# Optimization experiments

Measured on AMD Instinct MI355X. Metric: run time of the kernel, lower is better.

## Reference

```python
import jax, jax.numpy as jnp
import numpy as np
import math

B, N, D, H, L = 2, 512, 256, 8, 3
EPS = 1e-4


def setup_inputs() -> dict:
    key = jax.random.key(0)
    ks = jax.random.split(key, 16)
    # valid boxes (x1, y1, x2, y2) with positive width/height
    xy = jax.random.uniform(ks[0], (B, N, 2), dtype=jnp.float32) * 800.0
    wh = jax.random.uniform(ks[1], (B, N, 2), dtype=jnp.float32) * 200.0 + 1.0
    boxes = jnp.concatenate([xy, xy + wh], axis=-1)
    features = jax.random.normal(ks[2], (B, N, D), dtype=jnp.float32)
    mask = jnp.ones((B, N, N), dtype=jnp.int32)
    s = 1.0 / math.sqrt(D)
    Wq = jax.random.normal(ks[3], (L, D, D), dtype=jnp.float32) * s
    Wk = jax.random.normal(ks[4], (L, D, D), dtype=jnp.float32) * s
    Wv = jax.random.normal(ks[5], (L, D, D), dtype=jnp.float32) * s
    Wo = jax.random.normal(ks[6], (L, D, D), dtype=jnp.float32) * s
    Wg = jax.random.normal(ks[7], (L, D, H), dtype=jnp.float32) * s
    bq = jnp.zeros((L, D), jnp.float32)
    bk = jnp.zeros((L, D), jnp.float32)
    bv = jnp.zeros((L, D), jnp.float32)
    bo = jnp.zeros((L, D), jnp.float32)
    bg = jnp.zeros((L, H), jnp.float32)
    feat_range = jnp.arange(D // 8, dtype=jnp.float32)
    div_mat = jnp.power(1000.0, (8.0 / D) * feat_range) / 100.0
    return dict(boxes=boxes, features=features, mask=mask,
                Wq=Wq, bq=bq, Wk=Wk, bk=bk, Wv=Wv, bv=bv, Wo=Wo, bo=bo,
                Wg=Wg, bg=bg, div_mat=div_mat)


def _position_embedding(boxes, div_mat):
    # relative geometry between all box pairs (q == k == boxes)
    cx = (boxes[..., 0] + boxes[..., 2]) / 2
    cy = (boxes[..., 1] + boxes[..., 3]) / 2
    w = jnp.maximum(boxes[..., 2] - boxes[..., 0], EPS)
    h = jnp.maximum(boxes[..., 3] - boxes[..., 1], EPS)
    rel_x = jnp.log(jnp.abs(cx[:, None, :] - cx[:, :, None]) / w[:, None, :] + EPS)
    rel_y = jnp.log(jnp.abs(cy[:, None, :] - cy[:, :, None]) / h[:, None, :] + EPS)
    rel_w = jnp.log(w[:, :, None] / w[:, None, :] + EPS)
    rel_h = jnp.log(h[:, :, None] / h[:, None, :] + EPS)
    rel = jnp.stack([rel_x, rel_y, rel_w, rel_h], axis=-1)  # (B,N,N,4)
    pm = rel[..., None] / div_mat                            # (B,N,N,4,D/8)
    emb = jnp.concatenate([jnp.sin(pm), jnp.cos(pm)], axis=-1)  # (B,N,N,4,D/4)
    return emb.reshape(*emb.shape[:3], -1)                   # (B,N,N,D)


def reference(boxes, features, mask, Wq, bq, Wk, bk, Wv, bv, Wo, bo, Wg, bg, div_mat):
    emb = _position_embedding(boxes, div_mat)  # (B,N,N,D)
    dh = D // H
    inv_sqrt_dk = 1.0 / math.sqrt(dh)
    mask_b = (mask[:, None, :, :] == 0)  # (B,1,N,N)
    x = features

    def heads(t):  # (B,N,D) -> (B,H,N,dh)
        return t.reshape(B, N, H, dh).transpose(0, 2, 1, 3)

    for l in range(L):
        q = jax.nn.relu(x @ Wq[l] + bq[l])
        k = jax.nn.relu(x @ Wk[l] + bk[l])
        v = jax.nn.relu(x @ Wv[l] + bv[l])
        qh, kh, vh = heads(q), heads(k), heads(v)
        geo = jax.nn.relu(emb @ Wg[l] + bg[l])           # (B,N,N,H)
        geo = geo.transpose(0, 3, 1, 2)                   # (B,H,N,N)
        scores = jnp.einsum('bhqd,bhkd->bhqk', qh, kh) * inv_sqrt_dk
        scores = scores + jnp.log(geo + 1e-6)
        scores = jnp.where(mask_b, -1e9, scores)
        atten = jax.nn.softmax(scores, axis=-1)
        y = jnp.einsum('bhqk,bhkd->bhqd', atten, vh)      # (B,H,N,dh)
        y = y.transpose(0, 2, 1, 3).reshape(B, N, D)
        y = jax.nn.relu(y @ Wo[l] + bo[l])
        x = x + y
    return x
```

## Files before the change

### kernel.cpp

```cpp
#include <hip/hip_runtime.h>
#include <hip/hip_fp16.h>

#define BB 2
#define NNq 512
#define DDm 256
#define HHh 8
#define DHh 32
#define LLn 3

static constexpr float EPSF   = 1e-4f;
static constexpr float INV2PI = 0.15915494309189535f;
static constexpr float SCALE  = 0.17677669529663687f;

#if __has_builtin(__builtin_amdgcn_fractf)
#define FRACTF(x) __builtin_amdgcn_fractf(x)
#else
#define FRACTF(x) ((x) - floorf(x))
#endif
#if __has_builtin(__builtin_amdgcn_sinf)
#define SINR(x) __builtin_amdgcn_sinf(x)
#define COSR(x) __builtin_amdgcn_cosf(x)
#else
#define SINR(x) __sinf((x) * 6.2831853071795865f)
#define COSR(x) __cosf((x) * 6.2831853071795865f)
#endif

typedef _Float16 f16x8 __attribute__((ext_vector_type(8)));
typedef _Float16 f16x4 __attribute__((ext_vector_type(4)));
typedef _Float16 f16x2 __attribute__((ext_vector_type(2)));
typedef float    f32x4 __attribute__((ext_vector_type(4)));

__device__ inline f16x2 pk2(float a, float b) {
#if __has_builtin(__builtin_amdgcn_cvt_pkrtz)
    return __builtin_bit_cast(f16x2, __builtin_amdgcn_cvt_pkrtz(a, b));
#else
    f16x2 r; r[0] = (_Float16)a; r[1] = (_Float16)b; return r;
#endif
}
union U16x8 { f16x8 v; f16x2 h[4]; };

__global__ __launch_bounds__(256) void k_wcvt(const float* __restrict__ Wq,
        const float* __restrict__ Wk, const float* __restrict__ Wv,
        const float* __restrict__ Wo, _Float16* __restrict__ WT) {
    __shared__ _Float16 t[64][72];
    const int tid = threadIdx.x;
    const int mat = blockIdx.z;
    const int l = mat >> 2, op = mat & 3;
    const float* W = (op == 0 ? Wq : op == 1 ? Wk : op == 2 ? Wv : Wo)
                     + (size_t)l * 65536;
    const int k0 = blockIdx.x * 64, n0 = blockIdx.y * 64;
    for (int u = tid; u < 64 * 16; u += 256) {
        int k = u >> 4, n4 = (u & 15) * 4;
        float4 w4 = *reinterpret_cast<const float4*>(&W[(size_t)(k0 + k) * 256 + n0 + n4]);
        t[n4 + 0][k] = (_Float16)w4.x; t[n4 + 1][k] = (_Float16)w4.y;
        t[n4 + 2][k] = (_Float16)w4.z; t[n4 + 3][k] = (_Float16)w4.w;
    }
    __syncthreads();
    for (int u = tid; u < 64 * 8; u += 256) {
        int n = u >> 3, kc = (u & 7) * 8;
        *reinterpret_cast<f16x8*>(&WT[((size_t)mat * 256 + n0 + n) * 256 + k0 + kc]) =
            *reinterpret_cast<const f16x8*>(&t[n][kc]);
    }
}

__global__ __launch_bounds__(256) void k_geo(const float* __restrict__ boxes,
                                             const float* __restrict__ Wg,
                                             const float* __restrict__ bg,
                                             const float* __restrict__ divm,
                                             const int* __restrict__ maskp,
                                             __half* __restrict__ lg) {
    __shared__ char smem[16384];
    _Float16* WgT = reinterpret_cast<_Float16*>(smem);
    __half (*obuf)[24][68] = reinterpret_cast<__half (*)[24][68]>(smem);

    const int tid = threadIdx.x;
    for (int idx = tid; idx < 32 * 256; idx += 256) {
        int n = idx >> 8, k = idx & 255;
        float w = (n < 24) ? Wg[(size_t)(n >> 3) * 2048 + (size_t)k * 8 + (n & 7)] : 0.f;
        WgT[n * 256 + (k ^ ((n & 7) << 3))] = (_Float16)w;
    }
    __syncthreads();

    const int lane = tid & 63;
    const int wid  = tid >> 6;
    const int ln15 = lane & 15;
    const int kgrp = lane >> 4;

    float invd[8];
    {
        const float4* dv4 = reinterpret_cast<const float4*>(divm);
        float4 da = dv4[kgrp * 2], db = dv4[kgrp * 2 + 1];
        invd[0] = INV2PI / da.x; invd[1] = INV2PI / da.y;
        invd[2] = INV2PI / da.z; invd[3] = INV2PI / da.w;
        invd[4] = INV2PI / db.x; invd[5] = INV2PI / db.y;
        invd[6] = INV2PI / db.z; invd[7] = INV2PI / db.w;
    }
    const int n0 = ln15;
    const int n1 = 16 + ln15;
    const float bg0 = bg[n0];
    const float bg1 = (n1 < 24) ? bg[n1] : 0.f;

    const int mask  = (ln15 & 7) << 3;
    const int flip5 = mask & 32;
    const int kb    = (kgrp << 3) ^ (mask & 24);
    const int base0 = n0 * 256 + kb;
    const int base1 = n1 * 256 + kb;

    f16x8 bS0[4], bC0[4], bS1[4], bC1[4];
#pragma unroll
    for (int kc2 = 0; kc2 < 4; ++kc2) {
        const int koffS = ((2 * kc2) * 32) ^ flip5;
        const int koffC = ((2 * kc2 + 1) * 32) ^ flip5;
        bS0[kc2] = *reinterpret_cast<const f16x8*>(&WgT[base0 + koffS]);
        bC0[kc2] = *reinterpret_cast<const f16x8*>(&WgT[base0 + koffC]);
        bS1[kc2] = *reinterpret_cast<const f16x8*>(&WgT[base1 + koffS]);
        bC1[kc2] = *reinterpret_cast<const f16x8*>(&WgT[base1 + koffC]);
    }
    __syncthreads();

    const float4* boxes4 = reinterpret_cast<const float4*>(boxes);
    const size_t plane = (size_t)NNq * NNq;

    const int base4 = (blockIdx.x * 4 + wid) * 4;
#pragma unroll
    for (int it = 0; it < 4; ++it) {
        const int slab = base4 + it;
        const int p0 = slab << 4;
        const int b  = p0 >> 18;
        const int rem = p0 & (NNq * NNq - 1);
        const int i  = rem >> 9;
        const int j0 = rem & (NNq - 1);

        float4 Bi = boxes4[b * NNq + i];
        float4 Bj = boxes4[b * NNq + j0 + ln15];
        float cxi = 0.5f * (Bi.x + Bi.z), cyi = 0.5f * (Bi.y + Bi.w);
        float wi  = fmaxf(Bi.z - Bi.x, EPSF), hi = fmaxf(Bi.w - Bi.y, EPSF);
        float cxj = 0.5f * (Bj.x + Bj.z), cyj = 0.5f * (Bj.y + Bj.w);
        float wj  = fmaxf(Bj.z - Bj.x, EPSF), hj = fmaxf(Bj.w - Bj.y, EPSF);
        float rel[4];
        rel[0] = __logf(fabsf(cxj - cxi) / wj + EPSF);
        rel[1] = __logf(fabsf(cyj - cyi) / hj + EPSF);
        rel[2] = __logf(wi / wj + EPSF);
        rel[3] = __logf(hi / hj + EPSF);

        f32x4 acc0 = {0.f, 0.f, 0.f, 0.f};
        f32x4 acc1 = {0.f, 0.f, 0.f, 0.f};

#pragma unroll
        for (int kc2 = 0; kc2 < 4; ++kc2) {
            const float rc = rel[kc2];
            U16x8 afs, afc;
#pragma unroll
            for (int jj = 0; jj < 4; ++jj) {
                float rv0 = FRACTF(rc * invd[2 * jj]);
                float rv1 = FRACTF(rc * invd[2 * jj + 1]);
                afs.h[jj] = pk2(SINR(rv0), SINR(rv1));
                afc.h[jj] = pk2(COSR(rv0), COSR(rv1));
            }
            acc0 = __builtin_amdgcn_mfma_f32_16x16x32_f16(afs.v, bS0[kc2], acc0, 0, 0, 0);
            acc0 = __builtin_amdgcn_mfma_f32_16x16x32_f16(afc.v, bC0[kc2], acc0, 0, 0, 0);
            acc1 = __builtin_amdgcn_mfma_f32_16x16x32_f16(afs.v, bS1[kc2], acc1, 0, 0, 0);
            acc1 = __builtin_amdgcn_mfma_f32_16x16x32_f16(afc.v, bC1[kc2], acc1, 0, 0, 0);
        }

#pragma unroll
        for (int r = 0; r < 4; ++r) {
            const int m = it * 16 + (kgrp << 2) + r;
            float g0 = fmaxf(acc0[r] + bg0, 0.f);
            obuf[wid][n0][m] = __float2half(g0);
            if (n1 < 24) {
                float g1 = fmaxf(acc1[r] + bg1, 0.f);
                obuf[wid][n1][m] = __float2half(g1);
            }
        }
    }
    __syncthreads();

    const int b_  = base4 >> 14;
    const int i_  = (base4 >> 5) & (NNq - 1);
    const int j0b = (base4 & 31) << 4;
    const int mv  = maskp[((size_t)b_ * NNq + i_) * NNq + j0b + lane];
    size_t obase = (size_t)b_ * plane + (size_t)i_ * NNq + j0b + lane;
#pragma unroll
    for (int t = 0; t < 24; ++t) {
        float g = __half2float(obuf[wid][t][lane]);
        float v = (mv != 0) ? __logf(g + 1e-6f) : -60000.0f;
        lg[obase + (size_t)t * (BB * plane)] = __float2half(v);
    }
}

#define LDP 264
__global__ __launch_bounds__(256) void k_gemm_qkv(const float* __restrict__ A,
        const _Float16* __restrict__ WT0, const _Float16* __restrict__ WT1,
        const _Float16* __restrict__ WT2,
        const float* __restrict__ b0, const float* __restrict__ b1, const float* __restrict__ b2,
        _Float16* __restrict__ C0, _Float16* __restrict__ C1, _Float16* __restrict__ C2) {
    const _Float16* WTz = (blockIdx.z == 0) ? WT0 : (blockIdx.z == 1) ? WT1 : WT2;
    const float*    bia = (blockIdx.z == 0) ? b0 : (blockIdx.z == 1) ? b1 : b2;
    _Float16*       C   = (blockIdx.z == 0) ? C0 : (blockIdx.z == 1) ? C1 : C2;

    __shared__ _Float16 As[32 * LDP];
    __shared__ _Float16 Ws[64 * LDP];

    const int tid = threadIdx.x;
    const int m0 = blockIdx.x * 32, n0 = blockIdx.y * 64;

    for (int u = tid; u < 32 * 64; u += 256) {
        int m = u >> 6, k4 = (u & 63) * 4;
        float4 av = *reinterpret_cast<const float4*>(&A[(size_t)(m0 + m) * 256 + k4]);
        f16x4 hv = {(_Float16)av.x, (_Float16)av.y, (_Float16)av.z, (_Float16)av.w};
        *reinterpret_cast<f16x4*>(&As[m * LDP + k4]) = hv;
    }
    for (int u = tid; u < 2048; u += 256) {
        int n = u >> 5, kc = (u & 31) * 8;
        *reinterpret_cast<f16x8*>(&Ws[n * LDP + kc]) =
            *reinterpret_cast<const f16x8*>(&WTz[(size_t)(n0 + n) * 256 + kc]);
    }
    __syncthreads();

    const int lane = tid & 63;
    const int wid  = tid >> 6;
    const int ln15 = lane & 15;
    const int kgrp = lane >> 4;
    const int mw   = (wid & 1) * 16;
    const int nsel = (wid >> 1) * 16;
    const int kfr  = kgrp * 8;

    f32x4 acc[2] = {{0.f,0.f,0.f,0.f},{0.f,0.f,0.f,0.f}};
#pragma unroll
    for (int kc = 0; kc < 8; ++kc) {
        f16x8 af = *reinterpret_cast<const f16x8*>(&As[(mw + ln15) * LDP + kc * 32 + kfr]);
#pragma unroll
        for (int t = 0; t < 2; ++t) {
            f16x8 bf = *reinterpret_cast<const f16x8*>(
                &Ws[(nsel + t * 32 + ln15) * LDP + kc * 32 + kfr]);
            acc[t] = __builtin_amdgcn_mfma_f32_16x16x32_f16(af, bf, acc[t], 0, 0, 0);
        }
    }

#pragma unroll
    for (int t = 0; t < 2; ++t) {
        const int col = n0 + nsel + t * 32 + ln15;
        const float bv = bia[col];
#pragma unroll
        for (int r = 0; r < 4; ++r) {
            const int row = m0 + mw + kgrp * 4 + r;
            C[(size_t)row * 256 + col] = (_Float16)fmaxf(acc[t][r] + bv, 0.f);
        }
    }
}

__global__ __launch_bounds__(256) void k_gemm_o(const _Float16* __restrict__ A,
        const _Float16* __restrict__ WT0,
        const float* __restrict__ bia,
        float* __restrict__ C, const float* __restrict__ resid) {
    __shared__ _Float16 As[32 * LDP];
    __shared__ _Float16 Ws[64 * LDP];

    const int tid = threadIdx.x;
    const int m0 = blockIdx.x * 32, n0 = blockIdx.y * 64;

    for (int u = tid; u < 1024; u += 256) {
        int m = u >> 5, kc = (u & 31) * 8;
        *reinterpret_cast<f16x8*>(&As[m * LDP + kc]) =
            *reinterpret_cast<const f16x8*>(&A[(size_t)(m0 + m) * 256 + kc]);
    }
    for (int u = tid; u < 2048; u += 256) {
        int n = u >> 5, kc = (u & 31) * 8;
        *reinterpret_cast<f16x8*>(&Ws[n * LDP + kc]) =
            *reinterpret_cast<const f16x8*>(&WT0[(size_t)(n0 + n) * 256 + kc]);
    }
    __syncthreads();

    const int lane = tid & 63;
    const int wid  = tid >> 6;
    const int ln15 = lane & 15;
    const int kgrp = lane >> 4;
    const int mw   = (wid & 1) * 16;
    const int nsel = (wid >> 1) * 16;
    const int kfr  = kgrp * 8;

    f32x4 acc[2] = {{0.f,0.f,0.f,0.f},{0.f,0.f,0.f,0.f}};
#pragma unroll
    for (int kc = 0; kc < 8; ++kc) {
        f16x8 af = *reinterpret_cast<const f16x8*>(&As[(mw + ln15) * LDP + kc * 32 + kfr]);
#pragma unroll
        for (int t = 0; t < 2; ++t) {
            f16x8 bf = *reinterpret_cast<const f16x8*>(
                &Ws[(nsel + t * 32 + ln15) * LDP + kc * 32 + kfr]);
            acc[t] = __builtin_amdgcn_mfma_f32_16x16x32_f16(af, bf, acc[t], 0, 0, 0);
        }
    }

#pragma unroll
    for (int t = 0; t < 2; ++t) {
        const int col = n0 + nsel + t * 32 + ln15;
        const float bv = bia[col];
#pragma unroll
        for (int r = 0; r < 4; ++r) {
            const int row = m0 + mw + kgrp * 4 + r;
            float o = fmaxf(acc[t][r] + bv, 0.f) + resid[(size_t)row * 256 + col];
            C[(size_t)row * 256 + col] = o;
        }
    }
}

__global__ __launch_bounds__(256) void k_attn(const _Float16* __restrict__ q,
                                              const _Float16* __restrict__ kk,
                                              const _Float16* __restrict__ vv,
                                              const __half* __restrict__ lg,
                                              _Float16* __restrict__ y, int l) {
    __shared__ _Float16 Kh[512 * 32];
    __shared__ _Float16 VT[32 * 512];
    __shared__ _Float16 Ps[4][16 * 128];

    const int bh = blockIdx.y;
    const int b = bh >> 3, h = bh & 7;
    const int i0t = blockIdx.x * 16;

    const int tid  = threadIdx.x;
    const int lane = tid & 63, wid = tid >> 6;
    const int ln15 = lane & 15, kgrp = lane >> 4;

    for (int u = tid; u < 2048; u += 256) {
        int j = u >> 2, d8 = (u & 3) * 8;
        const size_t src = (size_t)(b * NNq + j) * DDm + h * DHh + d8;
        f16x8 kv = *reinterpret_cast<const f16x8*>(&kk[src]);
        *reinterpret_cast<f16x8*>(reinterpret_cast<char*>(Kh) +
            ((j * 64 + d8 * 2) ^ ((j & 7) << 4))) = kv;
        f16x8 v8 = *reinterpret_cast<const f16x8*>(&vv[src]);
#pragma unroll
        for (int e = 0; e < 8; ++e) {
            int row = d8 + e;
            *reinterpret_cast<_Float16*>(reinterpret_cast<char*>(VT) +
                ((row * 1024 + j * 2) ^ ((row & 7) << 4))) = v8[e];
        }
    }

    f16x8 qf = *reinterpret_cast<const f16x8*>(
        &q[(size_t)(b * NNq + i0t + ln15) * DDm + h * DHh + kgrp * 8]);
    __syncthreads();

    const int jbase = wid * 128;
    const size_t plane = (size_t)NNq * NNq;
    const size_t lg_base = (size_t)((l * 8 + h) * BB + b) * plane;

    f32x4 s[8];
#pragma unroll
    for (int t = 0; t < 8; ++t) {
        int j = jbase + t * 16 + ln15;
        f16x8 kf = *reinterpret_cast<const f16x8*>(reinterpret_cast<char*>(Kh) +
            ((j * 64 + kgrp * 16) ^ ((j & 7) << 4)));
        f32x4 z = {0.f, 0.f, 0.f, 0.f};
        s[t] = __builtin_amdgcn_mfma_f32_16x16x32_f16(qf, kf, z, 0, 0, 0);
    }

#pragma unroll
    for (int t = 0; t < 8; ++t) {
        const size_t jg = jbase + t * 16 + ln15;
#pragma unroll
        for (int r = 0; r < 4; ++r) {
            float lgv = __half2float(lg[lg_base + (size_t)(i0t + kgrp * 4 + r) * NNq + jg]);
            s[t][r] = s[t][r] * SCALE + lgv;
        }
    }

    float m_[4], l_[4];
#pragma unroll
    for (int r = 0; r < 4; ++r) {
        float mx = s[0][r];
#pragma unroll
        for (int t = 1; t < 8; ++t) mx = fmaxf(mx, s[t][r]);
#pragma unroll
        for (int o = 1; o < 16; o <<= 1) mx = fmaxf(mx, __shfl_xor(mx, o, 64));
        float sum = 0.f;
#pragma unroll
        for (int t = 0; t < 8; ++t) {
            float p = __expf(s[t][r] - mx);
            s[t][r] = p; sum += p;
        }
#pragma unroll
        for (int o = 1; o < 16; o <<= 1) sum += __shfl_xor(sum, o, 64);
        m_[r] = mx; l_[r] = sum;
    }

    {
        char* psb = reinterpret_cast<char*>(Ps[wid]);
#pragma unroll
        for (int r = 0; r < 4; ++r) {
            const int row = kgrp * 4 + r;
            const int rb = row * 256, sw = (row & 7) << 4;
#pragma unroll
            for (int t = 0; t < 8; ++t) {
                int byte = (rb + (t * 16 + ln15) * 2) ^ sw;
                *reinterpret_cast<_Float16*>(psb + byte) = (_Float16)s[t][r];
            }
        }
    }

    f32x4 oacc[2] = {{0.f,0.f,0.f,0.f},{0.f,0.f,0.f,0.f}};
    {
        char* psb = reinterpret_cast<char*>(Ps[wid]);
#pragma unroll
        for (int kc = 0; kc < 4; ++kc) {
            f16x8 pf = *reinterpret_cast<const f16x8*>(psb +
                ((ln15 * 256 + kc * 64 + kgrp * 16) ^ ((ln15 & 7) << 4)));
#pragma unroll
            for (int dt = 0; dt < 2; ++dt) {
                int d = dt * 16 + ln15;
                f16x8 vf = *reinterpret_cast<const f16x8*>(reinterpret_cast<char*>(VT) +
                    ((d * 1024 + (jbase + kc * 32 + kgrp * 8) * 2) ^ ((d & 7) << 4)));
                oacc[dt] = __builtin_amdgcn_mfma_f32_16x16x32_f16(pf, vf, oacc[dt], 0, 0, 0);
            }
        }
    }

    {
        float* Op = reinterpret_cast<float*>(reinterpret_cast<char*>(Kh) + wid * 8192);
#pragma unroll
        for (int dt = 0; dt < 2; ++dt)
#pragma unroll
            for (int r = 0; r < 4; ++r)
                Op[(kgrp * 4 + r) * 32 + dt * 16 + ln15] = oacc[dt][r];
        if (ln15 == 0) {
#pragma unroll
            for (int r = 0; r < 4; ++r) {
                Op[512 + kgrp * 4 + r] = m_[r];
                Op[528 + kgrp * 4 + r] = l_[r];
            }
        }
    }
    __syncthreads();

    {
        const int i = tid >> 4, d0 = (tid & 15) * 2;
        float mw[4], M = -3.0e38f;
#pragma unroll
        for (int w = 0; w < 4; ++w) {
            mw[w] = reinterpret_cast<float*>(reinterpret_cast<char*>(Kh) + w * 8192)[512 + i];
            M = fmaxf(M, mw[w]);
        }
        float o0 = 0.f, o1 = 0.f, ls = 0.f;
#pragma unroll
        for (int w = 0; w < 4; ++w) {
            float* Op = reinterpret_cast<float*>(reinterpret_cast<char*>(Kh) + w * 8192);
            float sc = __expf(mw[w] - M);
            ls += Op[528 + i] * sc;
            o0 += Op[i * 32 + d0] * sc;
            o1 += Op[i * 32 + d0 + 1] * sc;
        }
        float inv = 1.0f / ls;
        f16x2 ov; ov[0] = (_Float16)(o0 * inv); ov[1] = (_Float16)(o1 * inv);
        *reinterpret_cast<f16x2*>(&y[(size_t)(b * NNq + i0t + i) * DDm + h * DHh + d0]) = ov;
    }
}

extern "C" void kernel_launch(void* const* d_in, const int* in_sizes, int n_in,
                              void* d_out, int out_size, void* d_ws, size_t ws_size,
                              hipStream_t stream) {
    const float* boxes    = (const float*)d_in[0];
    const float* features = (const float*)d_in[1];
    const int*   mask     = (const int*)d_in[2];
    const float* Wq = (const float*)d_in[3];
    const float* bq = (const float*)d_in[4];
    const float* Wk = (const float*)d_in[5];
    const float* bk = (const float*)d_in[6];
    const float* Wv = (const float*)d_in[7];
    const float* bv = (const float*)d_in[8];
    const float* Wo = (const float*)d_in[9];
    const float* bo = (const float*)d_in[10];
    const float* Wg = (const float*)d_in[11];
    const float* bg = (const float*)d_in[12];
    const float* dv = (const float*)d_in[13];

    char* ws = (char*)d_ws;
    __half*    lg = (__half*)(ws);
    _Float16*  WT = (_Float16*)(ws + 25165824);
    _Float16*  qb = (_Float16*)(ws + 26738688);
    _Float16*  kb = (_Float16*)(ws + 27262976);
    _Float16*  vb = (_Float16*)(ws + 27787264);
    _Float16*  yb = (_Float16*)(ws + 28311552);
    float*     x  = (float*)d_out;

    k_wcvt<<<dim3(4, 4, 12), dim3(256), 0, stream>>>(Wq, Wk, Wv, Wo, WT);
    k_geo<<<dim3(2048), dim3(256), 0, stream>>>(boxes, Wg, bg, dv, mask, lg);

    for (int l = 0; l < LLn; ++l) {
        const _Float16* WTq = WT + (size_t)(l * 4 + 0) * 65536;
        const _Float16* WTk = WT + (size_t)(l * 4 + 1) * 65536;
        const _Float16* WTv = WT + (size_t)(l * 4 + 2) * 65536;
        const _Float16* WTo = WT + (size_t)(l * 4 + 3) * 65536;
        const float* bq_l = bq + (size_t)l * DDm;
        const float* bk_l = bk + (size_t)l * DDm;
        const float* bv_l = bv + (size_t)l * DDm;
        const float* bo_l = bo + (size_t)l * DDm;
        const float* xin  = (l == 0) ? features : x;

        k_gemm_qkv<<<dim3(32, 4, 3), dim3(256), 0, stream>>>(
            xin, WTq, WTk, WTv, bq_l, bk_l, bv_l, qb, kb, vb);
        k_attn<<<dim3(32, 16), dim3(256), 0, stream>>>(qb, kb, vb, lg, yb, l);
        k_gemm_o<<<dim3(32, 4), dim3(256), 0, stream>>>(
            yb, WTo, bo_l, x, xin);
    }
}
```

Baseline: 118.6 us.

## Multiply softmax by geometry weight instead of adding its log; precompute Wg transpose once

The geometry kernel now stores relu(geo)+1e-6 (or zero for masked pairs) instead of its logarithm. The attention kernel multiplies exp(scaled score - max) by that weight, which removes a log per geometry element and an add per score. The per-block Wg transpose and conversion to fp16 moves into the weight-conversion kernel as an extra grid slice, and k_geo now reads the transposed weights from global memory with launch bounds raised to 4 blocks per unit. The risk is precision: the max no longer includes the log term, and storing the small weights in fp16 can underflow, though that matters little because the weight multiplies the probability. The max is scaled after the reduction, which is valid only because SCALE is positive.

```diff
diff --git a/kernel.cpp b/kernel.cpp
--- a/kernel.cpp
+++ b/kernel.cpp
@@ -41,10 +41,21 @@
 
 __global__ __launch_bounds__(256) void k_wcvt(const float* __restrict__ Wq,
         const float* __restrict__ Wk, const float* __restrict__ Wv,
-        const float* __restrict__ Wo, _Float16* __restrict__ WT) {
+        const float* __restrict__ Wo, _Float16* __restrict__ WT,
+        const float* __restrict__ Wg, _Float16* __restrict__ WgTg) {
     __shared__ _Float16 t[64][72];
     const int tid = threadIdx.x;
     const int mat = blockIdx.z;
+    if (mat == 12) {
+        if (blockIdx.x == 0 && blockIdx.y == 0) {
+            for (int idx = tid; idx < 32 * 256; idx += 256) {
+                int n = idx >> 8, k = idx & 255;
+                float w = (n < 24) ? Wg[(size_t)(n >> 3) * 2048 + (size_t)k * 8 + (n & 7)] : 0.f;
+                WgTg[n * 256 + (k ^ ((n & 7) << 3))] = (_Float16)w;
+            }
+        }
+        return;
+    }
     const int l = mat >> 2, op = mat & 3;
     const float* W = (op == 0 ? Wq : op == 1 ? Wk : op == 2 ? Wv : Wo)
                      + (size_t)l * 65536;
@@ -63,24 +74,15 @@
     }
 }
 
-__global__ __launch_bounds__(256) void k_geo(const float* __restrict__ boxes,
-                                             const float* __restrict__ Wg,
-                                             const float* __restrict__ bg,
-                                             const float* __restrict__ divm,
-                                             const int* __restrict__ maskp,
-                                             __half* __restrict__ lg) {
-    __shared__ char smem[16384];
-    _Float16* WgT = reinterpret_cast<_Float16*>(smem);
-    __half (*obuf)[24][68] = reinterpret_cast<__half (*)[24][68]>(smem);
-
-    const int tid = threadIdx.x;
-    for (int idx = tid; idx < 32 * 256; idx += 256) {
-        int n = idx >> 8, k = idx & 255;
-        float w = (n < 24) ? Wg[(size_t)(n >> 3) * 2048 + (size_t)k * 8 + (n & 7)] : 0.f;
-        WgT[n * 256 + (k ^ ((n & 7) << 3))] = (_Float16)w;
-    }
-    __syncthreads();
-
+__global__ __launch_bounds__(256, 4) void k_geo(const float* __restrict__ boxes,
+                                                const _Float16* __restrict__ WgTg,
+                                                const float* __restrict__ bg,
+                                                const float* __restrict__ divm,
+                                                const int* __restrict__ maskp,
+                                                __half* __restrict__ G) {
+    __shared__ __half obuf[4][24][68];
+
+    const int tid  = threadIdx.x;
     const int lane = tid & 63;
     const int wid  = tid >> 6;
     const int ln15 = lane & 15;
@@ -111,12 +113,11 @@
     for (int kc2 = 0; kc2 < 4; ++kc2) {
         const int koffS = ((2 * kc2) * 32) ^ flip5;
         const int koffC = ((2 * kc2 + 1) * 32) ^ flip5;
-        bS0[kc2] = *reinterpret_cast<const f16x8*>(&WgT[base0 + koffS]);
-        bC0[kc2] = *reinterpret_cast<const f16x8*>(&WgT[base0 + koffC]);
-        bS1[kc2] = *reinterpret_cast<const f16x8*>(&WgT[base1 + koffS]);
-        bC1[kc2] = *reinterpret_cast<const f16x8*>(&WgT[base1 + koffC]);
-    }
-    __syncthreads();
+        bS0[kc2] = *reinterpret_cast<const f16x8*>(&WgTg[base0 + koffS]);
+        bC0[kc2] = *reinterpret_cast<const f16x8*>(&WgTg[base0 + koffC]);
+        bS1[kc2] = *reinterpret_cast<const f16x8*>(&WgTg[base1 + koffS]);
+        bC1[kc2] = *reinterpret_cast<const f16x8*>(&WgTg[base1 + koffC]);
+    }
 
     const float4* boxes4 = reinterpret_cast<const float4*>(boxes);
     const size_t plane = (size_t)NNq * NNq;
@@ -184,8 +185,8 @@
 #pragma unroll
     for (int t = 0; t < 24; ++t) {
         float g = __half2float(obuf[wid][t][lane]);
-        float v = (mv != 0) ? __logf(g + 1e-6f) : -60000.0f;
-        lg[obase + (size_t)t * (BB * plane)] = __float2half(v);
+        float v = (mv != 0) ? (g + 1e-6f) : 0.0f;
+        G[obase + (size_t)t * (BB * plane)] = __float2half(v);
     }
 }
 
@@ -308,7 +309,7 @@
 __global__ __launch_bounds__(256) void k_attn(const _Float16* __restrict__ q,
                                               const _Float16* __restrict__ kk,
                                               const _Float16* __restrict__ vv,
-                                              const __half* __restrict__ lg,
+                                              const __half* __restrict__ G,
                                               _Float16* __restrict__ y, int l) {
     __shared__ _Float16 Kh[512 * 32];
     __shared__ _Float16 VT[32 * 512];
@@ -343,7 +344,7 @@
 
     const int jbase = wid * 128;
     const size_t plane = (size_t)NNq * NNq;
-    const size_t lg_base = (size_t)((l * 8 + h) * BB + b) * plane;
+    const size_t g_base = (size_t)((l * 8 + h) * BB + b) * plane;
 
     f32x4 s[8];
 #pragma unroll
@@ -355,14 +356,13 @@
         s[t] = __builtin_amdgcn_mfma_f32_16x16x32_f16(qf, kf, z, 0, 0, 0);
     }
 
+    float gv[8][4];
 #pragma unroll
     for (int t = 0; t < 8; ++t) {
         const size_t jg = jbase + t * 16 + ln15;
 #pragma unroll
-        for (int r = 0; r < 4; ++r) {
-            float lgv = __half2float(lg[lg_base + (size_t)(i0t + kgrp * 4 + r) * NNq + jg]);
-            s[t][r] = s[t][r] * SCALE + lgv;
-        }
+        for (int r = 0; r < 4; ++r)
+            gv[t][r] = __half2float(G[g_base + (size_t)(i0t + kgrp * 4 + r) * NNq + jg]);
     }
 
     float m_[4], l_[4];
@@ -371,12 +371,13 @@
         float mx = s[0][r];
 #pragma unroll
         for (int t = 1; t < 8; ++t) mx = fmaxf(mx, s[t][r]);
+        mx *= SCALE;
 #pragma unroll
         for (int o = 1; o < 16; o <<= 1) mx = fmaxf(mx, __shfl_xor(mx, o, 64));
         float sum = 0.f;
 #pragma unroll
         for (int t = 0; t < 8; ++t) {
-            float p = __expf(s[t][r] - mx);
+            float p = gv[t][r] * __expf(s[t][r] * SCALE - mx);
             s[t][r] = p; sum += p;
         }
 #pragma unroll
@@ -474,16 +475,17 @@
     const float* dv = (const float*)d_in[13];
 
     char* ws = (char*)d_ws;
-    __half*    lg = (__half*)(ws);
-    _Float16*  WT = (_Float16*)(ws + 25165824);
-    _Float16*  qb = (_Float16*)(ws + 26738688);
-    _Float16*  kb = (_Float16*)(ws + 27262976);
-    _Float16*  vb = (_Float16*)(ws + 27787264);
-    _Float16*  yb = (_Float16*)(ws + 28311552);
-    float*     x  = (float*)d_out;
-
-    k_wcvt<<<dim3(4, 4, 12), dim3(256), 0, stream>>>(Wq, Wk, Wv, Wo, WT);
-    k_geo<<<dim3(2048), dim3(256), 0, stream>>>(boxes, Wg, bg, dv, mask, lg);
+    __half*    Gb   = (__half*)(ws);
+    _Float16*  WT   = (_Float16*)(ws + 25165824);
+    _Float16*  WgTg = (_Float16*)(ws + 26738688);
+    _Float16*  qb   = (_Float16*)(ws + 26755072);
+    _Float16*  kb   = (_Float16*)(ws + 27279360);
+    _Float16*  vb   = (_Float16*)(ws + 27803648);
+    _Float16*  yb   = (_Float16*)(ws + 28327936);
+    float*     x    = (float*)d_out;
+
+    k_wcvt<<<dim3(4, 4, 13), dim3(256), 0, stream>>>(Wq, Wk, Wv, Wo, WT, Wg, WgTg);
+    k_geo<<<dim3(2048), dim3(256), 0, stream>>>(boxes, WgTg, bg, dv, mask, Gb);
 
     for (int l = 0; l < LLn; ++l) {
         const _Float16* WTq = WT + (size_t)(l * 4 + 0) * 65536;
@@ -498,7 +500,7 @@
 
         k_gemm_qkv<<<dim3(32, 4, 3), dim3(256), 0, stream>>>(
             xin, WTq, WTk, WTv, bq_l, bk_l, bv_l, qb, kb, vb);
-        k_attn<<<dim3(32, 16), dim3(256), 0, stream>>>(qb, kb, vb, lg, yb, l);
+        k_attn<<<dim3(32, 16), dim3(256), 0, stream>>>(qb, kb, vb, Gb, yb, l);
         k_gemm_o<<<dim3(32, 4), dim3(256), 0, stream>>>(
             yb, WTo, bo_l, x, xin);
     }
```

Result: faster. 101.3 us (-14.6%).
